# Kernel tuning notes

Measured on AMD Instinct MI355X. Metric: run time of the kernel, lower is better.

The kernel has to match this reference:

```python
import jax, jax.numpy as jnp
import numpy as np

B, L, D, H = 2, 4096, 1024, 4
DV = D // H
NP = 5
MIN_PROB = 0.01
CHUNK = 32
RIN = D + H * NP * 4 + H * (NP * (NP - 1)) // 2  # 1144
RH = 2 * RIN


def dwconv_causal(x, w):
    # x: (B, L, C); w: (C, K) depthwise causal FIR
    K = w.shape[-1]
    xp = jnp.pad(x, ((0, 0), (K - 1, 0), (0, 0))).transpose(0, 2, 1)  # (B,C,L+K-1)
    y = jax.lax.conv_general_dilated(
        xp, w[:, None, :], window_strides=(1,), padding='VALID',
        feature_group_count=w.shape[0],
        dimension_numbers=('NCH', 'OIH', 'NCH'))
    return y.transpose(0, 2, 1)  # (B,L,C)


def l2norm(x):
    return x * jax.lax.rsqrt(jnp.sum(x * x, -1, keepdims=True) + 1e-12)


def delta_rule_chunkwise(q, k, v, beta, chunk=CHUNK):
    # q,k: (b,h,L,dk)  v: (b,h,L,dv)  beta: (b,h,L); L divisible by chunk
    b, h, Lq, dk = q.shape
    dv = v.shape[-1]
    n = Lq // chunk
    q = l2norm(q); k = l2norm(k)
    v = v * beta[..., None]
    kb = k * beta[..., None]
    r = lambda x: x.reshape(b, h, n, chunk, -1)
    q, k, v, kb = r(q), r(k), r(v), r(kb)
    tri = jnp.triu(jnp.ones((chunk, chunk), bool), 0)
    attn = jnp.where(tri, 0.0, -(kb @ jnp.swapaxes(k, -1, -2)))
    for i in range(1, chunk):  # in-chunk triangular-inverse recurrence
        upd = jnp.einsum('...k,...ki->...i', attn[..., i, :], attn[..., :, :i])
        attn = attn.at[..., i, :i].add(upd)
    attn = attn + jnp.eye(chunk, dtype=attn.dtype)
    u = attn @ v
    w = attn @ kb
    strict = jnp.triu(jnp.ones((chunk, chunk), bool), 1)

    def step(S, inp):
        qi, ki, ui, wi = inp
        la = jnp.where(strict, 0.0, qi @ jnp.swapaxes(ki, -1, -2))
        u_i = ui - wi @ S
        o_i = qi @ S + la @ u_i
        return S + jnp.swapaxes(ki, -1, -2) @ u_i, o_i

    mv = lambda x: jnp.moveaxis(x, 2, 0)
    S0 = jnp.zeros((b, h, dk, dv), q.dtype)
    S, o = jax.lax.scan(step, S0, (mv(q), mv(k), mv(u), mv(w)))
    return jnp.moveaxis(o, 0, 2).reshape(b, h, Lq, dv), S


def setup_inputs() -> dict:
    key = jax.random.key(0)
    ks = jax.random.split(key, 20)
    f = lambda k, shape, s=0.02: jax.random.normal(k, shape, jnp.float32) * s
    # FIR filters: identity tap (last) + small noise, matching learned-from-delta init
    def fir(k, ksz):
        w = np.zeros((D, ksz), np.float32)
        w[:, -1] = 1.0
        return jnp.asarray(w) + f(k, (D, ksz), 0.02)
    b2 = np.zeros((H, NP), np.float32)
    b2[:, -1] = 0.5
    b2[:, -2] = 0.5
    return {
        'hidden_states': jax.random.normal(ks[0], (B, L, D), jnp.float32),
        'Wq': f(ks[1], (D, D)), 'Wk': f(ks[2], (D, D)), 'Wv': f(ks[3], (D, D)),
        'wq_conv': f(ks[4], (D, 4), 0.2), 'wk_conv': f(ks[5], (D, 4), 0.2),
        'wv_conv': f(ks[6], (D, 4), 0.2),
        'Wb': f(ks[7], (H, D)),
        'fir_s_w': fir(ks[8], 3), 'fir_m_w': fir(ks[9], 7),
        'fir_l_w': fir(ks[10], 25), 'fir_id_w': fir(ks[11], 1),
        'W1': f(ks[12], (RH, RIN)), 'b1': jnp.zeros((RH,), jnp.float32),
        'W2': f(ks[13], (H * NP, RH)), 'b2': jnp.asarray(b2.reshape(-1)),
        'norm_w': jnp.ones((DV,), jnp.float32),
        'Wo': f(ks[14], (D, D)),
    }


def reference(hidden_states, Wq, Wk, Wv, wq_conv, wk_conv, wv_conv, Wb,
              fir_s_w, fir_m_w, fir_l_w, fir_id_w, W1, b1, W2, b2, norm_w, Wo):
    silu = jax.nn.silu
    q = silu(dwconv_causal(hidden_states @ Wq.T, wq_conv))
    k = silu(dwconv_causal(hidden_states @ Wk.T, wk_conv))
    v = silu(dwconv_causal(hidden_states @ Wv.T, wv_conv))
    beta = jax.nn.sigmoid(hidden_states @ Wb.T)  # (B,L,H)
    q4 = q.reshape(B, L, H, -1).transpose(0, 2, 1, 3)
    k4 = k.reshape(B, L, H, -1).transpose(0, 2, 1, 3)
    v4 = v.reshape(B, L, H, -1).transpose(0, 2, 1, 3)
    delta_out, _ = delta_rule_chunkwise(q4, k4, v4, beta.transpose(0, 2, 1))
    delta_out = delta_out.transpose(0, 2, 1, 3)  # (B,L,H,DV)
    fir = lambda w: dwconv_causal(v, w).reshape(B, L, H, DV)
    branches = [fir(fir_s_w), fir(fir_m_w), fir(fir_l_w), delta_out, fir(fir_id_w)]
    feats = []
    for x in branches:
        sm = jax.nn.softmax(x, -1)
        feats += [x.mean(-1), jnp.var(x, -1, ddof=1), jnp.max(x, -1),
                  -(sm * jnp.log(sm + 1e-8)).sum(-1)]
    cross = []
    for i in range(NP):
        for j in range(i + 1, NP):
            xi, xj = branches[i], branches[j]
            den = jnp.sqrt(jnp.sum(xi * xi, -1)) * jnp.sqrt(jnp.sum(xj * xj, -1)) + 1e-8
            cross.append(jnp.sum(xi * xj, -1) / den)
    router_in = jnp.concatenate([hidden_states] + feats + cross, axis=-1)  # (B,L,RIN)
    hrt = jax.nn.gelu(router_in @ W1.T + b1, approximate=False)
    logits = (hrt @ W2.T + b2).reshape(B, L, H, NP)
    p = jax.nn.softmax(logits, -1)
    p = p * (1.0 - NP * MIN_PROB) + MIN_PROB  # probability floor
    out = jnp.einsum('blhp,pblhd->blhd', p, jnp.stack(branches))
    out = out * jax.lax.rsqrt(jnp.mean(out * out, -1, keepdims=True) + 1e-5) * norm_w
    return out.reshape(B, L, H * DV) @ Wo.T
```

## Files before the change

kernel.cpp:

```cpp
#include <hip/hip_runtime.h>
#include <stdint.h>

typedef unsigned short u16t;
typedef u16t us4 __attribute__((ext_vector_type(4)));
typedef u16t us8 __attribute__((ext_vector_type(8)));
typedef __bf16 bf8v __attribute__((ext_vector_type(8)));
typedef float f4 __attribute__((ext_vector_type(4)));

#define MFMA(a, b, c) __builtin_amdgcn_mfma_f32_16x16x32_bf16((a), (b), (c), 0, 0, 0)

__device__ __forceinline__ float bf2f(u16t u) {
  union { unsigned int i; float f; } c; c.i = ((unsigned int)u) << 16; return c.f;
}
__device__ __forceinline__ u16t f2bf(float f) {
  union { float f; unsigned int i; } c; c.f = f;
  return (u16t)((c.i + 0x7FFFu + ((c.i >> 16) & 1u)) >> 16);
}
__device__ __forceinline__ float wsum(float v) {
#pragma unroll
  for (int o = 32; o > 0; o >>= 1) v += __shfl_xor(v, o);
  return v;
}
__device__ __forceinline__ float wmax(float v) {
#pragma unroll
  for (int o = 32; o > 0; o >>= 1) v = fmaxf(v, __shfl_xor(v, o));
  return v;
}

template <bool AF32, bool BF32, bool CF32>
__device__ __forceinline__ void gemm_body(const void* __restrict__ Av,
    const void* __restrict__ Btv, void* __restrict__ Cv,
    int K, int lda, int ldb, int ldc, int m0, int n0) {
  __shared__ u16t As[128][40];
  __shared__ u16t Bs[128][40];
  const int tid = threadIdx.x;
  const int wv = tid >> 6, l = tid & 63;
  const int wr = wv >> 1, wc = wv & 1;
  const int lr = l & 15, kg8 = (l >> 4) * 8, rg4 = (l >> 4) * 4;
  const int row_s = tid >> 1, seg = (tid & 1) * 16;
  const f4 zf = {0.f, 0.f, 0.f, 0.f};
  f4 acc[4][4];
#pragma unroll
  for (int i = 0; i < 4; ++i)
#pragma unroll
    for (int j = 0; j < 4; ++j) acc[i][j] = zf;

  for (int kt = 0; kt < K; kt += 32) {
    us8 a0, a1, b0, b1;
    if (AF32) {
      const float* pa = (const float*)Av + (size_t)(m0 + row_s) * lda + seg + kt;
      f4 fa0 = *(const f4*)(pa), fa1 = *(const f4*)(pa + 4);
      f4 fa2 = *(const f4*)(pa + 8), fa3 = *(const f4*)(pa + 12);
#pragma unroll
      for (int e = 0; e < 4; ++e) {
        a0[e] = f2bf(fa0[e]); a0[e + 4] = f2bf(fa1[e]);
        a1[e] = f2bf(fa2[e]); a1[e + 4] = f2bf(fa3[e]);
      }
    } else {
      const u16t* pa = (const u16t*)Av + (size_t)(m0 + row_s) * lda + seg + kt;
      a0 = *(const us8*)(pa); a1 = *(const us8*)(pa + 8);
    }
    if (BF32) {
      const float* pb = (const float*)Btv + (size_t)(n0 + row_s) * ldb + seg + kt;
      f4 fb0 = *(const f4*)(pb), fb1 = *(const f4*)(pb + 4);
      f4 fb2 = *(const f4*)(pb + 8), fb3 = *(const f4*)(pb + 12);
#pragma unroll
      for (int e = 0; e < 4; ++e) {
        b0[e] = f2bf(fb0[e]); b0[e + 4] = f2bf(fb1[e]);
        b1[e] = f2bf(fb2[e]); b1[e + 4] = f2bf(fb3[e]);
      }
    } else {
      const u16t* pb = (const u16t*)Btv + (size_t)(n0 + row_s) * ldb + seg + kt;
      b0 = *(const us8*)(pb); b1 = *(const us8*)(pb + 8);
    }
    *(us8*)&As[row_s][seg] = a0;
    *(us8*)&As[row_s][seg + 8] = a1;
    *(us8*)&Bs[row_s][seg] = b0;
    *(us8*)&Bs[row_s][seg + 8] = b1;
    __syncthreads();
    bf8v af[4], bg[4];
#pragma unroll
    for (int f = 0; f < 4; ++f) af[f] = *(const bf8v*)&As[wr * 64 + f * 16 + lr][kg8];
#pragma unroll
    for (int f = 0; f < 4; ++f) bg[f] = *(const bf8v*)&Bs[wc * 64 + f * 16 + lr][kg8];
#pragma unroll
    for (int i = 0; i < 4; ++i)
#pragma unroll
      for (int j = 0; j < 4; ++j) acc[i][j] = MFMA(af[i], bg[j], acc[i][j]);
    __syncthreads();
  }
#pragma unroll
  for (int i = 0; i < 4; ++i) {
    const int rb = m0 + wr * 64 + i * 16 + rg4;
#pragma unroll
    for (int j = 0; j < 4; ++j) {
      const int cb = n0 + wc * 64 + j * 16 + lr;
#pragma unroll
      for (int r = 0; r < 4; ++r) {
        if (CF32)
          ((float*)Cv)[(size_t)(rb + r) * ldc + cb] = acc[i][j][r];
        else
          ((u16t*)Cv)[(size_t)(rb + r) * ldc + cb] = f2bf(acc[i][j][r]);
      }
    }
  }
}

template <bool AF32, bool BF32, bool CF32>
__global__ __launch_bounds__(256) void gemm_bt(const void* __restrict__ Av,
    const void* __restrict__ Btv, void* __restrict__ Cv,
    int K, int lda, int ldb, int ldc) {
  gemm_body<AF32, BF32, CF32>(Av, Btv, Cv, K, lda, ldb, ldc,
                              blockIdx.y * 128, blockIdx.x * 128);
}

__global__ __launch_bounds__(256) void gemm_qkv3(const float* __restrict__ A,
    const float* __restrict__ B0, const float* __restrict__ B1,
    const float* __restrict__ B2, u16t* __restrict__ C0, u16t* __restrict__ C1,
    u16t* __restrict__ C2v) {
  const int z = blockIdx.z;
  const float* Bt = (z == 0) ? B0 : ((z == 1) ? B1 : B2);
  u16t* C = (z == 0) ? C0 : ((z == 1) ? C1 : C2v);
  gemm_body<true, true, false>(A, Bt, C, 1024, 1024, 1024, 1024,
                               blockIdx.y * 128, blockIdx.x * 128);
}

__global__ __launch_bounds__(256) void conv4_silu(
    const u16t* __restrict__ qlin, const u16t* __restrict__ klin, const u16t* __restrict__ vlin,
    const float* __restrict__ wq, const float* __restrict__ wk, const float* __restrict__ wvv,
    u16t* __restrict__ qc, u16t* __restrict__ kc, u16t* __restrict__ vc) {
  const int tid = threadIdx.x;
  const int l0 = blockIdx.x * 64;
  const int b = blockIdx.y >> 2, cb = blockIdx.y & 3;
  const int z = blockIdx.z;
  const u16t* in_ = (z == 0) ? qlin : ((z == 1) ? klin : vlin);
  const float* w_ = (z == 0) ? wq : ((z == 1) ? wk : wvv);
  u16t* out_ = (z == 0) ? qc : ((z == 1) ? kc : vc);
  const int c = cb * 256 + tid;
  __shared__ u16t sm[67][256];
  for (int i = 0; i < 67; ++i) {
    int ls = l0 - 3 + i;
    sm[i][tid] = (ls >= 0) ? in_[((size_t)b * 4096 + ls) * 1024 + c] : (u16t)0;
  }
  __syncthreads();
  f4 w4 = *(const f4*)&w_[c * 4];
  for (int ll = 0; ll < 64; ++ll) {
    float y = bf2f(sm[ll][tid]) * w4[0] + bf2f(sm[ll + 1][tid]) * w4[1] +
              bf2f(sm[ll + 2][tid]) * w4[2] + bf2f(sm[ll + 3][tid]) * w4[3];
    y = y / (1.f + expf(-y));
    out_[((size_t)b * 4096 + l0 + ll) * 1024 + c] = f2bf(y);
  }
}

__global__ __launch_bounds__(256) void beta_kernel(const float* __restrict__ hid,
    const float* __restrict__ Wb, float* __restrict__ beta) {
  const int m = blockIdx.x, tid = threadIdx.x;
  const int h = tid >> 6, l = tid & 63;
  float acc = 0.f;
#pragma unroll
  for (int it = 0; it < 4; ++it) {
    int kk = l * 4 + it * 256;
    f4 hv = *(const f4*)&hid[(size_t)m * 1024 + kk];
    f4 wv4 = *(const f4*)&Wb[(size_t)h * 1024 + kk];
#pragma unroll
    for (int e = 0; e < 4; ++e) acc += hv[e] * wv4[e];
  }
  acc = wsum(acc);
  if (l == 0) beta[m * 4 + h] = 1.f / (1.f + expf(-acc));
}

__global__ __launch_bounds__(256) void prep_kernel(u16t* __restrict__ qc, u16t* __restrict__ kc,
    const u16t* __restrict__ vc, const float* __restrict__ beta,
    u16t* __restrict__ kbeta, u16t* __restrict__ vbeta) {
  const int m = blockIdx.x, tid = threadIdx.x;
  const int h = tid >> 6, l = tid & 63;
  const size_t base = (size_t)m * 1024 + h * 256 + l * 4;
  const float bet = beta[m * 4 + h];
  us4 q4 = *(const us4*)&qc[base];
  float qf[4]; float ss = 0.f;
#pragma unroll
  for (int e = 0; e < 4; ++e) { qf[e] = bf2f(q4[e]); ss += qf[e] * qf[e]; }
  float qsc = rsqrtf(wsum(ss) + 1e-12f);
  us4 qo;
#pragma unroll
  for (int e = 0; e < 4; ++e) qo[e] = f2bf(qf[e] * qsc);
  *(us4*)&qc[base] = qo;
  us4 k4 = *(const us4*)&kc[base];
  float kf[4]; ss = 0.f;
#pragma unroll
  for (int e = 0; e < 4; ++e) { kf[e] = bf2f(k4[e]); ss += kf[e] * kf[e]; }
  float ksc = rsqrtf(wsum(ss) + 1e-12f);
  us4 ko, kbo;
#pragma unroll
  for (int e = 0; e < 4; ++e) {
    float kn = kf[e] * ksc;
    ko[e] = f2bf(kn);
    kbo[e] = f2bf(kn * bet);
  }
  *(us4*)&kc[base] = ko;
  *(us4*)&kbeta[base] = kbo;
  us4 v4 = *(const us4*)&vc[base];
  us4 vo;
#pragma unroll
  for (int e = 0; e < 4; ++e) vo[e] = f2bf(bf2f(v4[e]) * bet);
  *(us4*)&vbeta[base] = vo;
}

__global__ __launch_bounds__(256) void chunk_uw(const u16t* __restrict__ kn,
    const u16t* __restrict__ kbeta, const u16t* __restrict__ vbeta,
    u16t* __restrict__ ug, u16t* __restrict__ wg) {
  const int tid = threadIdx.x;
  const int bh = blockIdx.x >> 7, ci = blockIdx.x & 127;
  const int b = bh >> 2, h = bh & 3;
  const int l0 = ci * 32;
  __shared__ u16t kns[32][264], kbs[32][264], vbs[32][264];
  __shared__ float attn_s[32][33];
  const int sr = tid >> 5, sd8 = (tid & 31) * 8;
  const size_t rowbase = (size_t)b * 4096 * 1024 + (size_t)h * 256;
#pragma unroll
  for (int i = 0; i < 4; ++i) {
    int r = i * 8 + sr;
    size_t g = rowbase + (size_t)(l0 + r) * 1024 + sd8;
    *(us8*)&kns[r][sd8] = *(const us8*)&kn[g];
    *(us8*)&kbs[r][sd8] = *(const us8*)&kbeta[g];
    *(us8*)&vbs[r][sd8] = *(const us8*)&vbeta[g];
  }
  __syncthreads();
  {
    const int i = tid >> 3, j4 = (tid & 7) * 4;
    float d0 = 0.f, d1 = 0.f, d2 = 0.f, d3 = 0.f;
    for (int d8 = 0; d8 < 256; d8 += 8) {
      us8 kb8 = *(const us8*)&kbs[i][d8];
      us8 n0v = *(const us8*)&kns[j4][d8];
      us8 n1v = *(const us8*)&kns[j4 + 1][d8];
      us8 n2v = *(const us8*)&kns[j4 + 2][d8];
      us8 n3v = *(const us8*)&kns[j4 + 3][d8];
#pragma unroll
      for (int e = 0; e < 8; ++e) {
        float kv = bf2f(kb8[e]);
        d0 += kv * bf2f(n0v[e]); d1 += kv * bf2f(n1v[e]);
        d2 += kv * bf2f(n2v[e]); d3 += kv * bf2f(n3v[e]);
      }
    }
    attn_s[i][j4]     = (j4     < i) ? -d0 : 0.f;
    attn_s[i][j4 + 1] = (j4 + 1 < i) ? -d1 : 0.f;
    attn_s[i][j4 + 2] = (j4 + 2 < i) ? -d2 : 0.f;
    attn_s[i][j4 + 3] = (j4 + 3 < i) ? -d3 : 0.f;
  }
  __syncthreads();
  if (tid < 32) {
    const int j = tid;
    for (int i = 1; i < 32; ++i) {
      float aij = attn_s[i][j];
      float upd = 0.f;
#pragma unroll 1
      for (int k = 1; k < 31; ++k) {
        float aik = __shfl(aij, k);
        float akj = (k > j && k < i) ? attn_s[k][j] : 0.f;
        upd += aik * akj;
      }
      if (j < i) attn_s[i][j] = aij + upd;
    }
    attn_s[j][j] = 1.f;
  }
  __syncthreads();
  {
    const int r = tid >> 3, cg = (tid & 7) * 32;
    float ua[32], wa[32];
#pragma unroll
    for (int e = 0; e < 32; ++e) { ua[e] = 0.f; wa[e] = 0.f; }
    for (int j = 0; j < 32; ++j) {
      float a = attn_s[r][j];
#pragma unroll
      for (int e0 = 0; e0 < 32; e0 += 8) {
        us8 v8 = *(const us8*)&vbs[j][cg + e0];
        us8 k8 = *(const us8*)&kbs[j][cg + e0];
#pragma unroll
        for (int e = 0; e < 8; ++e) {
          ua[e0 + e] += a * bf2f(v8[e]);
          wa[e0 + e] += a * bf2f(k8[e]);
        }
      }
    }
    const size_t ob = ((size_t)bh * 4096 + l0 + r) * 256 + cg;
#pragma unroll
    for (int e0 = 0; e0 < 32; e0 += 8) {
      us8 pu, pw;
#pragma unroll
      for (int e = 0; e < 8; ++e) { pu[e] = f2bf(ua[e0 + e]); pw[e] = f2bf(wa[e0 + e]); }
      *(us8*)&ug[ob + e0] = pu;
      *(us8*)&wg[ob + e0] = pw;
    }
  }
}

__global__ __launch_bounds__(256, 1) void delta_scan(const u16t* __restrict__ qn,
    const u16t* __restrict__ kn, const u16t* __restrict__ ug, const u16t* __restrict__ wg,
    u16t* __restrict__ dout) {
  const int blk = blockIdx.x;
  const int bh = blk >> 2, vbidx = blk & 3;
  const int b = bh >> 2, h = bh & 3;
  const int c0 = vbidx * 64;
  const int tid = threadIdx.x;
  const int wv = tid >> 6, l = tid & 63;
  const int lr = l & 15, kg8 = (l >> 4) * 8, rg4 = (l >> 4) * 4;

  __shared__ u16t qs[32][264], ks2[32][264], wss[32][264];
  __shared__ u16t kts[256][40];
  __shared__ u16t sbf[64][264];
  __shared__ u16t las[32][40];
  __shared__ u16t uts[64][40];

  {
    u16t* sp = &sbf[0][0];
    for (int i = tid; i < 64 * 264; i += 256) sp[i] = 0;
  }
  const f4 zf = {0.f, 0.f, 0.f, 0.f};
  f4 sacc[16];
#pragma unroll
  for (int d = 0; d < 16; ++d) sacc[d] = zf;
  __syncthreads();

  const u16t* qb = qn + (size_t)b * 4096 * 1024 + (size_t)h * 256;
  const u16t* knb = kn + (size_t)b * 4096 * 1024 + (size_t)h * 256;
  const u16t* ub = ug + (size_t)bh * 4096 * 256;
  const u16t* wb = wg + (size_t)bh * 4096 * 256;
  const int sr = tid >> 5, sd8 = (tid & 31) * 8;

  us8 pq[4], pk[4], pw[4];
  us4 pu0, pu1;
  {
#pragma unroll
    for (int i = 0; i < 4; ++i) {
      const int r = i * 8 + sr;
      pq[i] = *(const us8*)(qb + (size_t)r * 1024 + sd8);
      pk[i] = *(const us8*)(knb + (size_t)r * 1024 + sd8);
      pw[i] = *(const us8*)(wb + (size_t)r * 256 + sd8);
    }
    pu0 = *(const us4*)(ub + (size_t)lr * 256 + c0 + wv * 16 + rg4);
    pu1 = *(const us4*)(ub + (size_t)(16 + lr) * 256 + c0 + wv * 16 + rg4);
  }

  for (int ci = 0; ci < 128; ++ci) {
    const int l0 = ci * 32;
#pragma unroll
    for (int i = 0; i < 4; ++i) {
      const int r = i * 8 + sr;
      *(us8*)&qs[r][sd8] = pq[i];
      *(us8*)&ks2[r][sd8] = pk[i];
      *(us8*)&wss[r][sd8] = pw[i];
    }
    const us4 u0 = pu0, u1 = pu1;
    __syncthreads();
    if (ci < 127) {
      const int l1 = l0 + 32;
#pragma unroll
      for (int i = 0; i < 4; ++i) {
        const int r = i * 8 + sr;
        pq[i] = *(const us8*)(qb + (size_t)(l1 + r) * 1024 + sd8);
        pk[i] = *(const us8*)(knb + (size_t)(l1 + r) * 1024 + sd8);
        pw[i] = *(const us8*)(wb + (size_t)(l1 + r) * 256 + sd8);
      }
      pu0 = *(const us4*)(ub + (size_t)(l1 + lr) * 256 + c0 + wv * 16 + rg4);
      pu1 = *(const us4*)(ub + (size_t)(l1 + 16 + lr) * 256 + c0 + wv * 16 + rg4);
    }
    {
      const int dk = tid;
      const int swz = ((dk >> 3) & 3) << 3;
#pragma unroll
      for (int r = 0; r < 32; r += 2) {
        unsigned int lo = ks2[r][dk], hi = ks2[r + 1][dk];
        *(unsigned int*)&kts[dk][r ^ swz] = lo | (hi << 16);
      }
    }
    {
      const int rq = wv >> 1, rk = wv & 1;
      f4 t4 = zf;
#pragma unroll
      for (int ks = 0; ks < 8; ++ks) {
        bf8v a = *(const bf8v*)&qs[rq * 16 + lr][ks * 32 + kg8];
        bf8v bb = *(const bf8v*)&ks2[rk * 16 + lr][ks * 32 + kg8];
        t4 = MFMA(a, bb, t4);
      }
      const int colj = rk * 16 + lr;
#pragma unroll
      for (int rr = 0; rr < 4; ++rr) {
        const int rowr = rq * 16 + rg4 + rr;
        las[rowr][colj] = (colj <= rowr) ? f2bf(t4[rr]) : (u16t)0;
      }
    }
    f4 o0 = zf, o1 = zf;
    {
      f4 m0 = zf, m1 = zf;
#pragma unroll
      for (int ks = 0; ks < 8; ++ks) {
        bf8v a = *(const bf8v*)&sbf[wv * 16 + lr][ks * 32 + kg8];
        bf8v wb0 = *(const bf8v*)&wss[lr][ks * 32 + kg8];
        bf8v wb1 = *(const bf8v*)&wss[16 + lr][ks * 32 + kg8];
        bf8v qb0 = *(const bf8v*)&qs[lr][ks * 32 + kg8];
        bf8v qb1 = *(const bf8v*)&qs[16 + lr][ks * 32 + kg8];
        m0 = MFMA(a, wb0, m0);
        m1 = MFMA(a, wb1, m1);
        o0 = MFMA(a, qb0, o0);
        o1 = MFMA(a, qb1, o1);
      }
#pragma unroll
      for (int rt = 0; rt < 2; ++rt) {
        f4 mm = rt ? m1 : m0;
        const us4 uu = rt ? u1 : u0;
        const int r = rt * 16 + lr;
#pragma unroll
        for (int rr = 0; rr < 4; ++rr)
          uts[wv * 16 + rg4 + rr][r] = f2bf(bf2f(uu[rr]) - mm[rr]);
      }
    }
    __syncthreads();
    {
      bf8v a2 = *(const bf8v*)&uts[wv * 16 + lr][kg8];
      {
        bf8v lb0 = *(const bf8v*)&las[lr][kg8];
        bf8v lb1 = *(const bf8v*)&las[16 + lr][kg8];
        o0 = MFMA(a2, lb0, o0);
        o1 = MFMA(a2, lb1, o1);
      }
#pragma unroll
      for (int rt = 0; rt < 2; ++rt) {
        f4 oo = rt ? o1 : o0;
        const int r = rt * 16 + lr;
        us4 st;
#pragma unroll
        for (int rr = 0; rr < 4; ++rr) st[rr] = f2bf(oo[rr]);
        *(us4*)(dout + ((size_t)(b * 4096 + l0 + r) * 4 + h) * 256 + c0 + wv * 16 + rg4) = st;
      }
#pragma unroll
      for (int d = 0; d < 16; ++d) {
        const int swzd = ((2 * d + (lr >> 3)) & 3) << 3;
        bf8v bb = *(const bf8v*)&kts[d * 16 + lr][kg8 ^ swzd];
        sacc[d] = MFMA(a2, bb, sacc[d]);
      }
#pragma unroll
      for (int d = 0; d < 16; ++d) {
#pragma unroll
        for (int rr = 0; rr < 4; ++rr)
          sbf[wv * 16 + rg4 + rr][d * 16 + lr] = f2bf(sacc[d][rr]);
      }
    }
    __syncthreads();
  }
}

__global__ __launch_bounds__(256) void fir_kernel(const u16t* __restrict__ vc,
    const float* __restrict__ w3g, const float* __restrict__ w7g,
    const float* __restrict__ w25g, const float* __restrict__ w1g,
    u16t* __restrict__ fs, u16t* __restrict__ fm, u16t* __restrict__ fl,
    u16t* __restrict__ fid) {
  const int tid = threadIdx.x;
  const int l0 = blockIdx.x * 64;
  const int b = blockIdx.y >> 2, cb = blockIdx.y & 3;
  const int c = cb * 256 + tid;
  __shared__ u16t sm[88][256];
  for (int i = 0; i < 88; ++i) {
    int ls = l0 - 24 + i;
    sm[i][tid] = (ls >= 0) ? vc[((size_t)b * 4096 + ls) * 1024 + c] : (u16t)0;
  }
  __syncthreads();
  float w3[3], w7[7], w25[25], w1_;
#pragma unroll
  for (int j = 0; j < 3; ++j) w3[j] = w3g[c * 3 + j];
#pragma unroll
  for (int j = 0; j < 7; ++j) w7[j] = w7g[c * 7 + j];
#pragma unroll
  for (int j = 0; j < 25; ++j) w25[j] = w25g[c * 25 + j];
  w1_ = w1g[c];
  for (int ll = 0; ll < 64; ++ll) {
    float x[25];
#pragma unroll
    for (int j = 0; j < 25; ++j) x[j] = bf2f(sm[ll + j][tid]);
    float ys = x[22] * w3[0] + x[23] * w3[1] + x[24] * w3[2];
    float ym = 0.f;
#pragma unroll
    for (int j = 0; j < 7; ++j) ym += x[18 + j] * w7[j];
    float yl = 0.f;
#pragma unroll
    for (int j = 0; j < 25; ++j) yl += x[j] * w25[j];
    float yi = x[24] * w1_;
    const size_t o = ((size_t)b * 4096 + l0 + ll) * 1024 + c;
    fs[o] = f2bf(ys); fm[o] = f2bf(ym); fl[o] = f2bf(yl); fid[o] = f2bf(yi);
  }
}

__global__ __launch_bounds__(256) void features_kernel(const float* __restrict__ hid,
    const u16t* __restrict__ p0, const u16t* __restrict__ p1, const u16t* __restrict__ p2,
    const u16t* __restrict__ p3, const u16t* __restrict__ p4, u16t* __restrict__ router) {
  const int m = blockIdx.x, tid = threadIdx.x;
  const int h = tid >> 6, l = tid & 63;
  const size_t base = (size_t)m * 1024 + h * 256 + l * 4;
  const u16t* bp[5] = {p0, p1, p2, p3, p4};
  float x[5][4];
#pragma unroll
  for (int br = 0; br < 5; ++br) {
    us4 v = *(const us4*)&bp[br][base];
#pragma unroll
    for (int e = 0; e < 4; ++e) x[br][e] = bf2f(v[e]);
  }
  float s1[5], s2[5], mx[5];
#pragma unroll
  for (int br = 0; br < 5; ++br) {
    float a = 0.f, bq = 0.f, m_ = -1e30f;
#pragma unroll
    for (int e = 0; e < 4; ++e) {
      a += x[br][e]; bq += x[br][e] * x[br][e]; m_ = fmaxf(m_, x[br][e]);
    }
    s1[br] = wsum(a); s2[br] = wsum(bq); mx[br] = wmax(m_);
  }
  float ent[5];
#pragma unroll
  for (int br = 0; br < 5; ++br) {
    float e_ = 0.f;
#pragma unroll
    for (int e = 0; e < 4; ++e) e_ += expf(x[br][e] - mx[br]);
    float es = wsum(e_);
    float hn = 0.f;
#pragma unroll
    for (int e = 0; e < 4; ++e) {
      float pv = expf(x[br][e] - mx[br]) / es;
      hn += pv * logf(pv + 1e-8f);
    }
    ent[br] = -wsum(hn);
  }
  float dt[10];
  {
    int pi = 0;
#pragma unroll
    for (int i = 0; i < 5; ++i)
#pragma unroll
      for (int j = i + 1; j < 5; ++j) {
        float d = 0.f;
#pragma unroll
        for (int e = 0; e < 4; ++e) d += x[i][e] * x[j][e];
        dt[pi] = wsum(d);
        ++pi;
      }
  }
  if (l == 0) {
    u16t* rp = router + (size_t)m * 1152 + 1024;
#pragma unroll
    for (int br = 0; br < 5; ++br) {
      float mean = s1[br] * (1.f / 256.f);
      float var = (s2[br] - s1[br] * s1[br] * (1.f / 256.f)) * (1.f / 255.f);
      rp[br * 16 + 0 + h] = f2bf(mean);
      rp[br * 16 + 4 + h] = f2bf(var);
      rp[br * 16 + 8 + h] = f2bf(mx[br]);
      rp[br * 16 + 12 + h] = f2bf(ent[br]);
    }
    int pi = 0;
#pragma unroll
    for (int i = 0; i < 5; ++i)
#pragma unroll
      for (int j = i + 1; j < 5; ++j) {
        float den = sqrtf(s2[i]) * sqrtf(s2[j]) + 1e-8f;
        rp[80 + pi * 4 + h] = f2bf(dt[pi] / den);
        ++pi;
      }
  }
  {
    f4 hv = *(const f4*)&hid[(size_t)m * 1024 + tid * 4];
    us4 hv4;
#pragma unroll
    for (int e = 0; e < 4; ++e) hv4[e] = f2bf(hv[e]);
    *(us4*)&router[(size_t)m * 1152 + tid * 4] = hv4;
  }
  if (tid < 8) router[(size_t)m * 1152 + 1144 + tid] = 0;
}

__global__ __launch_bounds__(256) void gelu_bias(u16t* __restrict__ hrt,
    const float* __restrict__ b1) {
  const size_t idx = ((size_t)blockIdx.x * 256 + threadIdx.x) * 4;
  const int col = (int)(idx % 2304);
  us4 v = *(const us4*)&hrt[idx];
  us4 o;
#pragma unroll
  for (int e = 0; e < 4; ++e) {
    int cc = col + e;
    float xx = bf2f(v[e]) + ((cc < 2288) ? b1[cc] : 0.f);
    float g = 0.5f * xx * (1.f + erff(xx * 0.70710678118f));
    o[e] = f2bf(g);
  }
  *(us4*)&hrt[idx] = o;
}

__global__ __launch_bounds__(256) void w2_softmax(const u16t* __restrict__ hrt,
    const float* __restrict__ W2, const float* __restrict__ b2, float* __restrict__ pout) {
  const int m = blockIdx.x, tid = threadIdx.x;
  const int h = tid >> 6, l = tid & 63;
  float acc[5];
#pragma unroll
  for (int n = 0; n < 5; ++n) acc[n] = 0.f;
  for (int kk = l * 4; kk < 2288; kk += 256) {
    us4 hv = *(const us4*)&hrt[(size_t)m * 2304 + kk];
    float hf[4];
#pragma unroll
    for (int e = 0; e < 4; ++e) hf[e] = bf2f(hv[e]);
#pragma unroll
    for (int n = 0; n < 5; ++n) {
      f4 wv4 = *(const f4*)&W2[(size_t)(h * 5 + n) * 2288 + kk];
#pragma unroll
      for (int e = 0; e < 4; ++e) acc[n] += hf[e] * wv4[e];
    }
  }
#pragma unroll
  for (int n = 0; n < 5; ++n) acc[n] = wsum(acc[n]);
  if (l == 0) {
    float lg[5];
#pragma unroll
    for (int n = 0; n < 5; ++n) lg[n] = acc[n] + b2[h * 5 + n];
    float mxv = lg[0];
#pragma unroll
    for (int n = 1; n < 5; ++n) mxv = fmaxf(mxv, lg[n]);
    float es = 0.f, ev[5];
#pragma unroll
    for (int n = 0; n < 5; ++n) { ev[n] = expf(lg[n] - mxv); es += ev[n]; }
#pragma unroll
    for (int n = 0; n < 5; ++n)
      pout[(size_t)m * 20 + h * 5 + n] = (ev[n] / es) * 0.95f + 0.01f;
  }
}

__global__ __launch_bounds__(256) void mix_kernel(const u16t* __restrict__ p0,
    const u16t* __restrict__ p1, const u16t* __restrict__ p2, const u16t* __restrict__ p3,
    const u16t* __restrict__ p4, const float* __restrict__ pbuf,
    const float* __restrict__ normw, u16t* __restrict__ mixed) {
  const int m = blockIdx.x, tid = threadIdx.x;
  const int h = tid >> 6, l = tid & 63;
  const size_t base = (size_t)m * 1024 + h * 256 + l * 4;
  const u16t* bp[5] = {p0, p1, p2, p3, p4};
  float p5[5];
#pragma unroll
  for (int n = 0; n < 5; ++n) p5[n] = pbuf[(size_t)m * 20 + h * 5 + n];
  float o[4] = {0.f, 0.f, 0.f, 0.f};
#pragma unroll
  for (int br = 0; br < 5; ++br) {
    us4 v = *(const us4*)&bp[br][base];
#pragma unroll
    for (int e = 0; e < 4; ++e) o[e] += p5[br] * bf2f(v[e]);
  }
  float ss = 0.f;
#pragma unroll
  for (int e = 0; e < 4; ++e) ss += o[e] * o[e];
  ss = wsum(ss);
  float sc = rsqrtf(ss * (1.f / 256.f) + 1e-5f);
  f4 nw = *(const f4*)&normw[l * 4];
  us4 ov;
#pragma unroll
  for (int e = 0; e < 4; ++e) ov[e] = f2bf(o[e] * sc * nw[e]);
  *(us4*)&mixed[base] = ov;
}

__global__ __launch_bounds__(256) void pad_w1(const float* __restrict__ W1,
    u16t* __restrict__ W1p) {
  size_t idx = (size_t)blockIdx.x * 256 + threadIdx.x;
  if (idx >= (size_t)2304 * 1152) return;
  int n = (int)(idx / 1152), k = (int)(idx % 1152);
  W1p[idx] = (n < 2288 && k < 1144) ? f2bf(W1[(size_t)n * 1144 + k]) : (u16t)0;
}

extern "C" void kernel_launch(void* const* d_in, const int* in_sizes, int n_in,
                              void* d_out, int out_size, void* d_ws, size_t ws_size,
                              hipStream_t stream) {
  (void)in_sizes; (void)n_in; (void)out_size; (void)ws_size;
  const float* hid = (const float*)d_in[0];
  const float* Wq = (const float*)d_in[1];
  const float* Wk = (const float*)d_in[2];
  const float* Wv = (const float*)d_in[3];
  const float* wqc = (const float*)d_in[4];
  const float* wkc = (const float*)d_in[5];
  const float* wvc = (const float*)d_in[6];
  const float* Wb = (const float*)d_in[7];
  const float* fsw = (const float*)d_in[8];
  const float* fmw = (const float*)d_in[9];
  const float* flw = (const float*)d_in[10];
  const float* fiw = (const float*)d_in[11];
  const float* W1 = (const float*)d_in[12];
  const float* b1 = (const float*)d_in[13];
  const float* W2 = (const float*)d_in[14];
  const float* b2 = (const float*)d_in[15];
  const float* nwt = (const float*)d_in[16];
  const float* Wo = (const float*)d_in[17];
  float* out = (float*)d_out;

  char* wsp = (char*)d_ws;
  const size_t S = (size_t)2 * 4096 * 1024 * 2;
  u16t* ql = (u16t*)(wsp + 0 * S);
  u16t* kl = (u16t*)(wsp + 1 * S);
  u16t* vl = (u16t*)(wsp + 2 * S);
  u16t* qc = (u16t*)(wsp + 3 * S);
  u16t* kc = (u16t*)(wsp + 4 * S);
  u16t* vc = (u16t*)(wsp + 5 * S);
  u16t* ubuf = (u16t*)(wsp + 6 * S);
  u16t* wbuf = (u16t*)(wsp + 7 * S);
  char* p = wsp + 8 * S;
  u16t* router = (u16t*)p; p += (size_t)8192 * 1152 * 2;
  u16t* hrt = (u16t*)p;    p += (size_t)8192 * 2304 * 2;
  u16t* w1p = (u16t*)p;    p += (size_t)2304 * 1152 * 2;
  float* pbuf = (float*)p; p += (size_t)8192 * 20 * 4;
  float* beta = (float*)p; p += (size_t)8192 * 4 * 4;
  u16t* kbeta = ql;
  u16t* vbeta = kl;
  u16t* dlt = kl;
  u16t* f_s = vl;
  u16t* f_m = qc;
  u16t* f_l = kc;
  u16t* f_i = ubuf;
  u16t* mixed = wbuf;

  dim3 blk(256);
  gemm_qkv3<<<dim3(8, 64, 3), blk, 0, stream>>>(hid, Wq, Wk, Wv, ql, kl, vl);
  conv4_silu<<<dim3(64, 8, 3), blk, 0, stream>>>(ql, kl, vl, wqc, wkc, wvc, qc, kc, vc);
  beta_kernel<<<dim3(8192), blk, 0, stream>>>(hid, Wb, beta);
  prep_kernel<<<dim3(8192), blk, 0, stream>>>(qc, kc, vc, beta, kbeta, vbeta);
  chunk_uw<<<dim3(1024), blk, 0, stream>>>(kc, kbeta, vbeta, ubuf, wbuf);
  delta_scan<<<dim3(32), blk, 0, stream>>>(qc, kc, ubuf, wbuf, dlt);
  fir_kernel<<<dim3(64, 8), blk, 0, stream>>>(vc, fsw, fmw, flw, fiw, f_s, f_m, f_l, f_i);
  features_kernel<<<dim3(8192), blk, 0, stream>>>(hid, f_s, f_m, f_l, dlt, f_i, router);
  pad_w1<<<dim3(10368), blk, 0, stream>>>(W1, w1p);
  gemm_bt<false, false, false><<<dim3(18, 64), blk, 0, stream>>>(router, w1p, hrt, 1152, 1152, 1152, 2304);
  gelu_bias<<<dim3(18432), blk, 0, stream>>>(hrt, b1);
  w2_softmax<<<dim3(8192), blk, 0, stream>>>(hrt, W2, b2, pbuf);
  mix_kernel<<<dim3(8192), blk, 0, stream>>>(f_s, f_m, f_l, dlt, f_i, pbuf, nwt, mixed);
  gemm_bt<false, true, true><<<dim3(8, 64), blk, 0, stream>>>(mixed, Wo, out, 1024, 1024, 1024, 1024);
}
```

Baseline: 1.136 ms.

## Widen delta scan blocks to 512 threads and slide FIR/conv register windows

The delta-rule scan now runs 16 blocks of 512 threads, each owning 128 value columns instead of 64. The shared q/k/w chunk staging and the key transpose are now shared across twice as many columns, and the next-chunk global prefetch moves after the mid-iteration barrier. The trailing per-chunk barrier is removed. Separately, the causal conv and FIR kernels keep a sliding register window so each step reads only one new shared-memory value. The wider block halves the number of scan blocks and so reduces parallelism on a latency-bound serial scan, and removing the end-of-loop barrier may open a race between the sbf writes and the next iteration's reads.

```diff
diff --git a/kernel.cpp b/kernel.cpp
--- a/kernel.cpp
+++ b/kernel.cpp
@@ -144,11 +144,13 @@
   }
   __syncthreads();
   f4 w4 = *(const f4*)&w_[c * 4];
+  float x0 = bf2f(sm[0][tid]), x1 = bf2f(sm[1][tid]), x2 = bf2f(sm[2][tid]);
   for (int ll = 0; ll < 64; ++ll) {
-    float y = bf2f(sm[ll][tid]) * w4[0] + bf2f(sm[ll + 1][tid]) * w4[1] +
-              bf2f(sm[ll + 2][tid]) * w4[2] + bf2f(sm[ll + 3][tid]) * w4[3];
+    float x3 = bf2f(sm[ll + 3][tid]);
+    float y = x0 * w4[0] + x1 * w4[1] + x2 * w4[2] + x3 * w4[3];
     y = y / (1.f + expf(-y));
     out_[((size_t)b * 4096 + l0 + ll) * 1024 + c] = f2bf(y);
+    x0 = x1; x1 = x2; x2 = x3;
   }
 }
 
@@ -294,26 +296,28 @@
   }
 }
 
-__global__ __launch_bounds__(256, 1) void delta_scan(const u16t* __restrict__ qn,
+__global__ __launch_bounds__(512, 2) void delta_scan(const u16t* __restrict__ qn,
     const u16t* __restrict__ kn, const u16t* __restrict__ ug, const u16t* __restrict__ wg,
     u16t* __restrict__ dout) {
   const int blk = blockIdx.x;
-  const int bh = blk >> 2, vbidx = blk & 3;
+  const int bh = blk >> 1, half = blk & 1;
   const int b = bh >> 2, h = bh & 3;
-  const int c0 = vbidx * 64;
+  const int c0 = half * 128;
   const int tid = threadIdx.x;
   const int wv = tid >> 6, l = tid & 63;
   const int lr = l & 15, kg8 = (l >> 4) * 8, rg4 = (l >> 4) * 4;
+  const int cw = c0 + wv * 16;
+  const int cl = wv * 16;
 
   __shared__ u16t qs[32][264], ks2[32][264], wss[32][264];
   __shared__ u16t kts[256][40];
-  __shared__ u16t sbf[64][264];
+  __shared__ u16t sbf[128][264];
   __shared__ u16t las[32][40];
-  __shared__ u16t uts[64][40];
+  __shared__ u16t uts[128][40];
 
   {
     u16t* sp = &sbf[0][0];
-    for (int i = tid; i < 64 * 264; i += 256) sp[i] = 0;
+    for (int i = tid; i < 128 * 264; i += 512) sp[i] = 0;
   }
   const f4 zf = {0.f, 0.f, 0.f, 0.f};
   f4 sacc[16];
@@ -327,53 +331,43 @@
   const u16t* wb = wg + (size_t)bh * 4096 * 256;
   const int sr = tid >> 5, sd8 = (tid & 31) * 8;
 
-  us8 pq[4], pk[4], pw[4];
+  us8 pq[2], pk[2], pw[2];
   us4 pu0, pu1;
   {
 #pragma unroll
-    for (int i = 0; i < 4; ++i) {
-      const int r = i * 8 + sr;
+    for (int i = 0; i < 2; ++i) {
+      const int r = sr + i * 16;
       pq[i] = *(const us8*)(qb + (size_t)r * 1024 + sd8);
       pk[i] = *(const us8*)(knb + (size_t)r * 1024 + sd8);
       pw[i] = *(const us8*)(wb + (size_t)r * 256 + sd8);
     }
-    pu0 = *(const us4*)(ub + (size_t)lr * 256 + c0 + wv * 16 + rg4);
-    pu1 = *(const us4*)(ub + (size_t)(16 + lr) * 256 + c0 + wv * 16 + rg4);
+    pu0 = *(const us4*)(ub + (size_t)lr * 256 + cw + rg4);
+    pu1 = *(const us4*)(ub + (size_t)(16 + lr) * 256 + cw + rg4);
   }
 
   for (int ci = 0; ci < 128; ++ci) {
     const int l0 = ci * 32;
 #pragma unroll
-    for (int i = 0; i < 4; ++i) {
-      const int r = i * 8 + sr;
+    for (int i = 0; i < 2; ++i) {
+      const int r = sr + i * 16;
       *(us8*)&qs[r][sd8] = pq[i];
       *(us8*)&ks2[r][sd8] = pk[i];
       *(us8*)&wss[r][sd8] = pw[i];
     }
     const us4 u0 = pu0, u1 = pu1;
     __syncthreads();
-    if (ci < 127) {
-      const int l1 = l0 + 32;
-#pragma unroll
-      for (int i = 0; i < 4; ++i) {
-        const int r = i * 8 + sr;
-        pq[i] = *(const us8*)(qb + (size_t)(l1 + r) * 1024 + sd8);
-        pk[i] = *(const us8*)(knb + (size_t)(l1 + r) * 1024 + sd8);
-        pw[i] = *(const us8*)(wb + (size_t)(l1 + r) * 256 + sd8);
-      }
-      pu0 = *(const us4*)(ub + (size_t)(l1 + lr) * 256 + c0 + wv * 16 + rg4);
-      pu1 = *(const us4*)(ub + (size_t)(l1 + 16 + lr) * 256 + c0 + wv * 16 + rg4);
-    }
     {
-      const int dk = tid;
+      const int dk = tid & 255;
+      const int rh = (tid >> 8) * 16;
       const int swz = ((dk >> 3) & 3) << 3;
 #pragma unroll
-      for (int r = 0; r < 32; r += 2) {
+      for (int rr = 0; rr < 16; rr += 2) {
+        const int r = rh + rr;
         unsigned int lo = ks2[r][dk], hi = ks2[r + 1][dk];
         *(unsigned int*)&kts[dk][r ^ swz] = lo | (hi << 16);
       }
     }
-    {
+    if (wv < 4) {
       const int rq = wv >> 1, rk = wv & 1;
       f4 t4 = zf;
 #pragma unroll
@@ -394,7 +388,7 @@
       f4 m0 = zf, m1 = zf;
 #pragma unroll
       for (int ks = 0; ks < 8; ++ks) {
-        bf8v a = *(const bf8v*)&sbf[wv * 16 + lr][ks * 32 + kg8];
+        bf8v a = *(const bf8v*)&sbf[cl + lr][ks * 32 + kg8];
         bf8v wb0 = *(const bf8v*)&wss[lr][ks * 32 + kg8];
         bf8v wb1 = *(const bf8v*)&wss[16 + lr][ks * 32 + kg8];
         bf8v qb0 = *(const bf8v*)&qs[lr][ks * 32 + kg8];
@@ -411,12 +405,24 @@
         const int r = rt * 16 + lr;
 #pragma unroll
         for (int rr = 0; rr < 4; ++rr)
-          uts[wv * 16 + rg4 + rr][r] = f2bf(bf2f(uu[rr]) - mm[rr]);
+          uts[cl + rg4 + rr][r] = f2bf(bf2f(uu[rr]) - mm[rr]);
       }
     }
     __syncthreads();
+    if (ci < 127) {
+      const int l1 = l0 + 32;
+#pragma unroll
+      for (int i = 0; i < 2; ++i) {
+        const int r = sr + i * 16;
+        pq[i] = *(const us8*)(qb + (size_t)(l1 + r) * 1024 + sd8);
+        pk[i] = *(const us8*)(knb + (size_t)(l1 + r) * 1024 + sd8);
+        pw[i] = *(const us8*)(wb + (size_t)(l1 + r) * 256 + sd8);
+      }
+      pu0 = *(const us4*)(ub + (size_t)(l1 + lr) * 256 + cw + rg4);
+      pu1 = *(const us4*)(ub + (size_t)(l1 + 16 + lr) * 256 + cw + rg4);
+    }
     {
-      bf8v a2 = *(const bf8v*)&uts[wv * 16 + lr][kg8];
+      bf8v a2 = *(const bf8v*)&uts[cl + lr][kg8];
       {
         bf8v lb0 = *(const bf8v*)&las[lr][kg8];
         bf8v lb1 = *(const bf8v*)&las[16 + lr][kg8];
@@ -430,7 +436,7 @@
         us4 st;
 #pragma unroll
         for (int rr = 0; rr < 4; ++rr) st[rr] = f2bf(oo[rr]);
-        *(us4*)(dout + ((size_t)(b * 4096 + l0 + r) * 4 + h) * 256 + c0 + wv * 16 + rg4) = st;
+        *(us4*)(dout + ((size_t)(b * 4096 + l0 + r) * 4 + h) * 256 + cw + rg4) = st;
       }
 #pragma unroll
       for (int d = 0; d < 16; ++d) {
@@ -442,10 +448,9 @@
       for (int d = 0; d < 16; ++d) {
 #pragma unroll
         for (int rr = 0; rr < 4; ++rr)
-          sbf[wv * 16 + rg4 + rr][d * 16 + lr] = f2bf(sacc[d][rr]);
-      }
-    }
-    __syncthreads();
+          sbf[cl + rg4 + rr][d * 16 + lr] = f2bf(sacc[d][rr]);
+      }
+    }
   }
 }
 
@@ -472,10 +477,10 @@
 #pragma unroll
   for (int j = 0; j < 25; ++j) w25[j] = w25g[c * 25 + j];
   w1_ = w1g[c];
+  float x[25];
+#pragma unroll
+  for (int j = 0; j < 25; ++j) x[j] = bf2f(sm[j][tid]);
   for (int ll = 0; ll < 64; ++ll) {
-    float x[25];
-#pragma unroll
-    for (int j = 0; j < 25; ++j) x[j] = bf2f(sm[ll + j][tid]);
     float ys = x[22] * w3[0] + x[23] * w3[1] + x[24] * w3[2];
     float ym = 0.f;
 #pragma unroll
@@ -486,6 +491,11 @@
     float yi = x[24] * w1_;
     const size_t o = ((size_t)b * 4096 + l0 + ll) * 1024 + c;
     fs[o] = f2bf(ys); fm[o] = f2bf(ym); fl[o] = f2bf(yl); fid[o] = f2bf(yi);
+    if (ll < 63) {
+#pragma unroll
+      for (int j = 0; j < 24; ++j) x[j] = x[j + 1];
+      x[24] = bf2f(sm[ll + 25][tid]);
+    }
   }
 }
 
@@ -719,7 +729,7 @@
   beta_kernel<<<dim3(8192), blk, 0, stream>>>(hid, Wb, beta);
   prep_kernel<<<dim3(8192), blk, 0, stream>>>(qc, kc, vc, beta, kbeta, vbeta);
   chunk_uw<<<dim3(1024), blk, 0, stream>>>(kc, kbeta, vbeta, ubuf, wbuf);
-  delta_scan<<<dim3(32), blk, 0, stream>>>(qc, kc, ubuf, wbuf, dlt);
+  delta_scan<<<dim3(16), dim3(512), 0, stream>>>(qc, kc, ubuf, wbuf, dlt);
   fir_kernel<<<dim3(64, 8), blk, 0, stream>>>(vc, fsw, fmw, flw, fiw, f_s, f_m, f_l, f_i);
   features_kernel<<<dim3(8192), blk, 0, stream>>>(hid, f_s, f_m, f_l, dlt, f_i, router);
   pad_w1<<<dim3(10368), blk, 0, stream>>>(W1, w1p);
```

After: 1.228 ms. +8.0%, slower.

## Pre-pack fp32 GEMM operands to bf16 and use sliding windows in convs

Applied to the files above, without the earlier changes.

Adds a pack_bf16 kernel that converts hidden states and the Wq/Wk/Wv/Wo weights to bf16 before the QKV and output GEMMs, so the GEMM tiles load half the bytes and skip per-tile conversion. It also makes the short conv and FIR kernels keep a sliding register window instead of re-reading every tap from shared memory at each position. The cost is five extra launches and an extra pass over the inputs and weights, and the packed buffers reuse workspace regions that later stages also use.

```diff
diff --git a/kernel.cpp b/kernel.cpp
--- a/kernel.cpp
+++ b/kernel.cpp
@@ -25,6 +25,17 @@
 #pragma unroll
   for (int o = 32; o > 0; o >>= 1) v = fmaxf(v, __shfl_xor(v, o));
   return v;
+}
+
+__global__ __launch_bounds__(256) void pack_bf16(const float* __restrict__ src,
+    u16t* __restrict__ dst, int n4) {
+  const int i = blockIdx.x * 256 + threadIdx.x;
+  if (i >= n4) return;
+  f4 v = *(const f4*)&src[(size_t)i * 4];
+  us4 o;
+#pragma unroll
+  for (int e = 0; e < 4; ++e) o[e] = f2bf(v[e]);
+  *(us4*)&dst[(size_t)i * 4] = o;
 }
 
 template <bool AF32, bool BF32, bool CF32>
@@ -114,15 +125,15 @@
                               blockIdx.y * 128, blockIdx.x * 128);
 }
 
-__global__ __launch_bounds__(256) void gemm_qkv3(const float* __restrict__ A,
-    const float* __restrict__ B0, const float* __restrict__ B1,
-    const float* __restrict__ B2, u16t* __restrict__ C0, u16t* __restrict__ C1,
+__global__ __launch_bounds__(256) void gemm_qkv3(const u16t* __restrict__ A,
+    const u16t* __restrict__ B0, const u16t* __restrict__ B1,
+    const u16t* __restrict__ B2, u16t* __restrict__ C0, u16t* __restrict__ C1,
     u16t* __restrict__ C2v) {
   const int z = blockIdx.z;
-  const float* Bt = (z == 0) ? B0 : ((z == 1) ? B1 : B2);
+  const u16t* Bt = (z == 0) ? B0 : ((z == 1) ? B1 : B2);
   u16t* C = (z == 0) ? C0 : ((z == 1) ? C1 : C2v);
-  gemm_body<true, true, false>(A, Bt, C, 1024, 1024, 1024, 1024,
-                               blockIdx.y * 128, blockIdx.x * 128);
+  gemm_body<false, false, false>(A, Bt, C, 1024, 1024, 1024, 1024,
+                                 blockIdx.y * 128, blockIdx.x * 128);
 }
 
 __global__ __launch_bounds__(256) void conv4_silu(
@@ -144,11 +155,13 @@
   }
   __syncthreads();
   f4 w4 = *(const f4*)&w_[c * 4];
+  float x0 = bf2f(sm[0][tid]), x1 = bf2f(sm[1][tid]), x2 = bf2f(sm[2][tid]);
   for (int ll = 0; ll < 64; ++ll) {
-    float y = bf2f(sm[ll][tid]) * w4[0] + bf2f(sm[ll + 1][tid]) * w4[1] +
-              bf2f(sm[ll + 2][tid]) * w4[2] + bf2f(sm[ll + 3][tid]) * w4[3];
+    float x3 = bf2f(sm[ll + 3][tid]);
+    float y = x0 * w4[0] + x1 * w4[1] + x2 * w4[2] + x3 * w4[3];
     y = y / (1.f + expf(-y));
     out_[((size_t)b * 4096 + l0 + ll) * 1024 + c] = f2bf(y);
+    x0 = x1; x1 = x2; x2 = x3;
   }
 }
 
@@ -472,10 +485,10 @@
 #pragma unroll
   for (int j = 0; j < 25; ++j) w25[j] = w25g[c * 25 + j];
   w1_ = w1g[c];
+  float x[25];
+#pragma unroll
+  for (int j = 0; j < 25; ++j) x[j] = bf2f(sm[j][tid]);
   for (int ll = 0; ll < 64; ++ll) {
-    float x[25];
-#pragma unroll
-    for (int j = 0; j < 25; ++j) x[j] = bf2f(sm[ll + j][tid]);
     float ys = x[22] * w3[0] + x[23] * w3[1] + x[24] * w3[2];
     float ym = 0.f;
 #pragma unroll
@@ -486,6 +499,11 @@
     float yi = x[24] * w1_;
     const size_t o = ((size_t)b * 4096 + l0 + ll) * 1024 + c;
     fs[o] = f2bf(ys); fm[o] = f2bf(ym); fl[o] = f2bf(yl); fid[o] = f2bf(yi);
+    if (ll < 63) {
+#pragma unroll
+      for (int j = 0; j < 24; ++j) x[j] = x[j + 1];
+      x[24] = bf2f(sm[ll + 25][tid]);
+    }
   }
 }
 
@@ -704,6 +722,10 @@
   u16t* w1p = (u16t*)p;    p += (size_t)2304 * 1152 * 2;
   float* pbuf = (float*)p; p += (size_t)8192 * 20 * 4;
   float* beta = (float*)p; p += (size_t)8192 * 4 * 4;
+  u16t* hidb = qc;
+  u16t* wqb = kc;
+  u16t* wkb = kc + 1048576;
+  u16t* wvb = kc + 2097152;
   u16t* kbeta = ql;
   u16t* vbeta = kl;
   u16t* dlt = kl;
@@ -712,9 +734,14 @@
   u16t* f_l = kc;
   u16t* f_i = ubuf;
   u16t* mixed = wbuf;
+  u16t* wob = w1p;
 
   dim3 blk(256);
-  gemm_qkv3<<<dim3(8, 64, 3), blk, 0, stream>>>(hid, Wq, Wk, Wv, ql, kl, vl);
+  pack_bf16<<<dim3(8192), blk, 0, stream>>>(hid, hidb, 2097152);
+  pack_bf16<<<dim3(1024), blk, 0, stream>>>(Wq, wqb, 262144);
+  pack_bf16<<<dim3(1024), blk, 0, stream>>>(Wk, wkb, 262144);
+  pack_bf16<<<dim3(1024), blk, 0, stream>>>(Wv, wvb, 262144);
+  gemm_qkv3<<<dim3(8, 64, 3), blk, 0, stream>>>(hidb, wqb, wkb, wvb, ql, kl, vl);
   conv4_silu<<<dim3(64, 8, 3), blk, 0, stream>>>(ql, kl, vl, wqc, wkc, wvc, qc, kc, vc);
   beta_kernel<<<dim3(8192), blk, 0, stream>>>(hid, Wb, beta);
   prep_kernel<<<dim3(8192), blk, 0, stream>>>(qc, kc, vc, beta, kbeta, vbeta);
@@ -727,5 +754,6 @@
   gelu_bias<<<dim3(18432), blk, 0, stream>>>(hrt, b1);
   w2_softmax<<<dim3(8192), blk, 0, stream>>>(hrt, W2, b2, pbuf);
   mix_kernel<<<dim3(8192), blk, 0, stream>>>(f_s, f_m, f_l, dlt, f_i, pbuf, nwt, mixed);
-  gemm_bt<false, true, true><<<dim3(8, 64), blk, 0, stream>>>(mixed, Wo, out, 1024, 1024, 1024, 1024);
-}
+  pack_bf16<<<dim3(1024), blk, 0, stream>>>(Wo, wob, 262144);
+  gemm_bt<false, false, true><<<dim3(8, 64), blk, 0, stream>>>(mixed, wob, out, 1024, 1024, 1024, 1024);
+}
```

New measurement: 1.099 ms. 1.03x faster.
